# Kernel optimization log

Hardware: AMD Instinct MI355X
Metric: run time of the kernel (lower is better)

The kernel has to match this reference:

```python
import jax, jax.numpy as jnp
import numpy as np

N, C, CI, H, W = 4, 512, 256, 64, 64  # batch, in_channels, inter_channels, spatial
EPS = 1e-5


def conv1x1(x, w, b):
    # x: (N,C,H,W), w: (O,C), b: (O,)
    return jnp.einsum('nchw,oc->nohw', x, w) + b[None, :, None, None]


def setup_inputs() -> dict:
    key = jax.random.key(0)
    ks = jax.random.split(key, 11)
    s = 0.02
    return {
        'x': jax.random.normal(ks[0], (N, C, H, W), dtype=jnp.float32),
        'g_w': jax.random.normal(ks[1], (CI, C), dtype=jnp.float32) * s,
        'g_b': jax.random.normal(ks[2], (CI,), dtype=jnp.float32) * s,
        'theta_w': jax.random.normal(ks[3], (CI, C), dtype=jnp.float32) * s,
        'theta_b': jax.random.normal(ks[4], (CI,), dtype=jnp.float32) * s,
        'phi_w': jax.random.normal(ks[5], (CI, C), dtype=jnp.float32) * s,
        'phi_b': jax.random.normal(ks[6], (CI,), dtype=jnp.float32) * s,
        'wz_w': jax.random.normal(ks[7], (C, CI), dtype=jnp.float32) * s,
        'wz_b': jax.random.normal(ks[8], (C,), dtype=jnp.float32) * s,
        'bn_gamma': jax.random.normal(ks[9], (C,), dtype=jnp.float32) * 0.1 + 1.0,
        'bn_beta': jax.random.normal(ks[10], (C,), dtype=jnp.float32) * 0.1,
    }


def reference(x, g_w, g_b, theta_w, theta_b, phi_w, phi_b, wz_w, wz_b, bn_gamma, bn_beta):
    # NLBlockND.forward_self, mode='embedded', dimension=2, bn_layer=True
    n = x.shape[0]
    L = x.shape[2] * x.shape[3]  # H*W tokens
    g_x = conv1x1(x, g_w, g_b).reshape(n, CI, L)          # (N,Ci,L)
    theta_x = conv1x1(x, theta_w, theta_b).reshape(n, CI, L)
    phi_x = conv1x1(x, phi_w, phi_b).reshape(n, CI, L)
    f = jnp.einsum('ncl,ncm->nlm', theta_x, phi_x)        # (N,L,L) = theta^T @ phi
    f_div_C = jax.nn.softmax(f, axis=-1)
    y = jnp.einsum('nlm,ncm->ncl', f_div_C, g_x)          # (N,Ci,L) = (attn @ g)^T
    y = y.reshape(n, CI, x.shape[2], x.shape[3])
    w_y = conv1x1(y, wz_w, wz_b)                          # (N,C,H,W)
    # BatchNorm2d, training-mode batch statistics (biased variance)
    mean = jnp.mean(w_y, axis=(0, 2, 3), keepdims=True)
    var = jnp.var(w_y, axis=(0, 2, 3), keepdims=True)
    w_y = (w_y - mean) * jax.lax.rsqrt(var + EPS)
    w_y = w_y * bn_gamma[None, :, None, None] + bn_beta[None, :, None, None]
    return w_y + x
```

## Files before the change

### kernel.cpp

```cpp
#include <hip/hip_runtime.h>
#include <hip/hip_bf16.h>
#include <hip/hip_fp16.h>


#define NB    4
#define CDIM  512
#define CIDIM 256
#define LDIM  4096
#define BN_EPS 1e-5f
#define LOG2E 1.4426950408889634f

typedef unsigned short u16;
typedef __attribute__((ext_vector_type(8))) short short8;
typedef __attribute__((ext_vector_type(4))) float f32x4;
typedef __attribute__((ext_vector_type(16))) float f32x16;

#define WY_OFF    0
#define THPH_OFF  8388608
#define G_OFF     12582912
#define Y_OFF     14680064
#define WTS_OFF   16777216
#define BIAS2_OFF 17039360
#define ML_OFF    17039872
#define ST_OFF    17105408

__device__ __forceinline__ u16 f2b(float f) {
    union { float f; unsigned u; } v; v.f = f;
    return (u16)((v.u + 0x7FFFu + ((v.u >> 16) & 1u)) >> 16);
}

__device__ __forceinline__ float b2f(u16 x) {
    return __uint_as_float((unsigned)x << 16);
}

__device__ __forceinline__ unsigned pack2(float a, float b) {
    return (unsigned)f2b(a) | ((unsigned)f2b(b) << 16);
}

__device__ __forceinline__ float fast_exp2(float x) {
#if __has_builtin(__builtin_amdgcn_exp2f)
    return __builtin_amdgcn_exp2f(x);
#else
    float r; asm("v_exp_f32 %0, %1" : "=v"(r) : "v"(x)); return r;
#endif
}

__device__ __forceinline__ void gl_lds16(const u16* g, u16* l) {
    __builtin_amdgcn_global_load_lds(
        (const __attribute__((address_space(1))) void*)g,
        (__attribute__((address_space(3))) void*)l, 16, 0, 0);
}

__global__ void transpose_x(const float* __restrict__ x, u16* __restrict__ xt) {
    __shared__ float tile[32][33];
    int n = blockIdx.z;
    int l0 = blockIdx.x * 32, c0 = blockIdx.y * 32;
    const float* xn = x + (size_t)n * CDIM * LDIM;
    u16* xtn = xt + (size_t)n * LDIM * CDIM;
    int tx = threadIdx.x, ty = threadIdx.y;
#pragma unroll
    for (int k = 0; k < 4; k++)
        tile[ty + 8 * k][tx] = xn[(size_t)(c0 + ty + 8 * k) * LDIM + l0 + tx];
    __syncthreads();
#pragma unroll
    for (int k = 0; k < 4; k++)
        xtn[(size_t)(l0 + ty + 8 * k) * CDIM + c0 + tx] = f2b(tile[tx][ty + 8 * k]);
}

__global__ void cast_w(const float* __restrict__ gw, const float* __restrict__ tw,
                       const float* __restrict__ pw, const float* __restrict__ zw,
                       u16* __restrict__ out,
                       const float* __restrict__ tb, const float* __restrict__ pb,
                       float* __restrict__ bc) {
    int idx = blockIdx.x * 256 + threadIdx.x;
    if (idx < 4 * 131072) {
        int seg = idx >> 17, off = idx & 131071;
        const float* s = (seg == 0) ? gw : (seg == 1) ? tw : (seg == 2) ? pw : zw;
        float v = s[off];
        if (seg == 1) v *= LOG2E;
        out[idx] = f2b(v);
    } else {
        int i = idx - 4 * 131072;
        if (i < 256) bc[i] = tb[i] * LOG2E;
        else if (i < 512) bc[i] = pb[i - 256];
    }
}

template <int BIAS_MODE, bool OUT_BF16>
__global__ __launch_bounds__(256)
void gemm_nt(const u16* __restrict__ A, const u16* __restrict__ B,
             void* __restrict__ Dv, const float* __restrict__ bias,
             int K, int lda, int ldb, int ldd,
             long batchA, long batchB, long batchD) {
    __shared__ __align__(16) u16 As[128 * 32];
    __shared__ __align__(16) u16 Bs[128 * 32];
    int z = blockIdx.z;
    A += (size_t)z * batchA;
    B += (size_t)z * batchB;

    int tid = threadIdx.x, lane = tid & 63, wave = tid >> 6;
    int n0 = blockIdx.x * 128, m0 = blockIdx.y * 128;
    int wr = wave >> 1, wc = wave & 1;

    f32x4 acc[4][4];
#pragma unroll
    for (int i = 0; i < 4; i++)
#pragma unroll
        for (int j = 0; j < 4; j++) acc[i][j] = (f32x4){0.f, 0.f, 0.f, 0.f};

    int sr = wave * 16 + (lane >> 2);
    int ss = ((lane & 3) ^ ((lane >> 2) & 3)) * 8;
    const u16* Ag0 = A + (size_t)(m0 + sr) * lda + ss;
    const u16* Ag1 = A + (size_t)(m0 + 64 + sr) * lda + ss;
    const u16* Bg0 = B + (size_t)(n0 + sr) * ldb + ss;
    const u16* Bg1 = B + (size_t)(n0 + 64 + sr) * ldb + ss;
    u16* Al0 = &As[(wave * 16) * 32];
    u16* Al1 = &As[(64 + wave * 16) * 32];
    u16* Bl0 = &Bs[(wave * 16) * 32];
    u16* Bl1 = &Bs[(64 + wave * 16) * 32];

    int koff = ((lane >> 4) ^ (lane & 3)) * 8;
    int ra = (wr * 64 + (lane & 15)) * 32 + koff;
    int rb = (wc * 64 + (lane & 15)) * 32 + koff;

    for (int k0 = 0; k0 < K; k0 += 32) {
        __syncthreads();
        gl_lds16(Ag0 + k0, Al0);
        gl_lds16(Ag1 + k0, Al1);
        gl_lds16(Bg0 + k0, Bl0);
        gl_lds16(Bg1 + k0, Bl1);
        __syncthreads();

        short8 af[4], bf[4];
#pragma unroll
        for (int mt = 0; mt < 4; mt++) af[mt] = *(const short8*)&As[ra + mt * 16 * 32];
#pragma unroll
        for (int nt = 0; nt < 4; nt++) bf[nt] = *(const short8*)&Bs[rb + nt * 16 * 32];
#pragma unroll
        for (int mt = 0; mt < 4; mt++)
#pragma unroll
            for (int nt = 0; nt < 4; nt++)
                acc[mt][nt] = __builtin_amdgcn_mfma_f32_16x16x32_bf16(
                    af[mt], bf[nt], acc[mt][nt], 0, 0, 0);
    }

#pragma unroll
    for (int mt = 0; mt < 4; mt++) {
        int mg = m0 + wr * 64 + mt * 16 + (lane >> 4) * 4;
#pragma unroll
        for (int nt = 0; nt < 4; nt++) {
            int ng = n0 + wc * 64 + nt * 16 + (lane & 15);
#pragma unroll
            for (int r = 0; r < 4; r++) {
                float v = acc[mt][nt][r];
                if (BIAS_MODE == 1) v += bias[mg + r];
                if (BIAS_MODE == 2) v += bias[ng];
                if (OUT_BF16) {
                    u16* D = (u16*)Dv + (size_t)z * batchD;
                    D[(size_t)(mg + r) * ldd + ng] = f2b(v);
                } else {
                    float* D = (float*)Dv + (size_t)z * batchD;
                    D[(size_t)(mg + r) * ldd + ng] = v;
                }
            }
        }
    }
}

__global__ __launch_bounds__(256, 2)
void flash_attn(const u16* __restrict__ THPH, const u16* __restrict__ G,
                u16* __restrict__ OPB, unsigned* __restrict__ ML4) {
    __shared__ __align__(16) u16 Ks[2][32 * 256];
    __shared__ __align__(16) u16 Vs[2][256 * 32];

    int b = blockIdx.x;
    int n = b & 3;
    int jh = (b >> 2) & 3;
    int qt = b >> 4;
    int q0 = qt * 128;

    const u16* TH = THPH + (size_t)n * LDIM * 512;
    const u16* PH = TH + 256;
    const u16* Gn = G + (size_t)n * LDIM * CIDIM;
    u16* OPh = OPB + ((size_t)jh * NB + n) * CIDIM * LDIM;
    unsigned* MLh = ML4 + ((size_t)jh * NB + n) * LDIM;

    int tid = threadIdx.x, lane = tid & 63, w = tid >> 6;
    int h = lane >> 5, lq = lane & 31, l7 = lane & 7;

    short8 qf[16];
    {
        const u16* qb = TH + (size_t)(q0 + w * 32 + lq) * 512 + h * 8;
#pragma unroll
        for (int c = 0; c < 16; c++) qf[c] = *(const short8*)(qb + c * 16);
    }

    f32x16 o[8];
#pragma unroll
    for (int i = 0; i < 8; i++)
#pragma unroll
        for (int e = 0; e < 16; e++) o[i][e] = 0.f;
    float m = -3e38f, lsum = 0.f;

    int krh = lane >> 5;
    int ksl = lane & 31;
    int vr = lane >> 2;
    int vsl = (lane & 3) ^ ((lane >> 3) & 3);

#define STAGE(bufi, jt_) do {                                                  \
    int j0_ = jh * 1024 + (jt_) * 32;                                          \
    _Pragma("unroll")                                                          \
    for (int i = 0; i < 4; i++) {                                              \
        int r = w * 8 + 2 * i + krh;                                           \
        int s = ksl ^ (r & 7);                                                 \
        gl_lds16(PH + (size_t)(j0_ + r) * 512 + s * 8,                         \
                 &Ks[bufi][(w * 8 + 2 * i) * 256]);                            \
    }                                                                          \
    _Pragma("unroll")                                                          \
    for (int i = 0; i < 4; i++) {                                              \
        int r = w * 64 + 16 * i + vr;                                          \
        gl_lds16(Gn + (size_t)r * LDIM + j0_ + vsl * 8,                        \
                 &Vs[bufi][(w * 64 + 16 * i) * 32]);                           \
    }                                                                          \
} while (0)

    STAGE(0, 0);
    int cur = 0;

#pragma unroll 1
    for (int jt = 0; jt < 32; jt++) {
        __syncthreads();
        if (jt + 1 < 32) STAGE(cur ^ 1, jt + 1);

        const u16* kb = Ks[cur];
        const u16* vb = Vs[cur];

        f32x16 sv;
#pragma unroll
        for (int e = 0; e < 16; e++) sv[e] = 0.f;
#pragma unroll
        for (int c = 0; c < 16; c++) {
            int slot = (c * 2 + h) ^ l7;
            short8 ka = *(const short8*)&kb[lq * 256 + slot * 8];
            sv = __builtin_amdgcn_mfma_f32_32x32x16_bf16(ka, qf[c], sv, 0, 0, 0);
        }

        float tm = sv[0];
#pragma unroll
        for (int r = 1; r < 16; r++) tm = fmaxf(tm, sv[r]);
        tm = fmaxf(tm, __shfl_xor(tm, 32, 64));

        if (!__all(tm <= m + 11.5f)) {
            float mnew = fmaxf(m, tm);
            float al = fast_exp2(m - mnew);
            m = mnew;
            lsum *= al;
#pragma unroll
            for (int i = 0; i < 8; i++)
#pragma unroll
                for (int e = 0; e < 16; e++) o[i][e] *= al;
        }

        float rs = 0.f;
#pragma unroll
        for (int r = 0; r < 16; r++) {
            float p = fast_exp2(sv[r] - m);
            sv[r] = p;
            rs += p;
        }
        lsum += rs + __shfl_xor(rs, 32, 64);

#pragma unroll
        for (int st = 0; st < 2; st++) {
            int r0 = 8 * st;
            float e0 = sv[r0 + 0], e1 = sv[r0 + 1];
            float e2 = sv[r0 + 2], e3 = sv[r0 + 3];
            float e4 = sv[r0 + 4], e5 = sv[r0 + 5];
            float e6 = sv[r0 + 6], e7 = sv[r0 + 7];
            unsigned own_a = h ? pack2(e4, e5) : pack2(e0, e1);
            unsigned own_b = h ? pack2(e6, e7) : pack2(e2, e3);
            unsigned snd_a = h ? pack2(e0, e1) : pack2(e4, e5);
            unsigned snd_b = h ? pack2(e2, e3) : pack2(e6, e7);
            unsigned rcv_a = __shfl_xor(snd_a, 32, 64);
            unsigned rcv_b = __shfl_xor(snd_b, 32, 64);
            union { unsigned u[4]; short8 v; } pf;
            pf.u[0] = h ? rcv_a : own_a;
            pf.u[1] = h ? rcv_b : own_b;
            pf.u[2] = h ? own_a : rcv_a;
            pf.u[3] = h ? own_b : rcv_b;
            int slot = (st * 2 + h) ^ ((lq >> 1) & 3);
#pragma unroll
            for (int cit = 0; cit < 8; cit++) {
                short8 va = *(const short8*)&vb[(cit * 32 + lq) * 32 + slot * 8];
                o[cit] = __builtin_amdgcn_mfma_f32_32x32x16_bf16(va, pf.v, o[cit], 0, 0, 0);
            }
        }
        cur ^= 1;
    }

    int q = q0 + w * 32 + lq;
    if (h == 0) {
        unsigned pm = (unsigned)__half_as_ushort(__float2half(m));
        unsigned pl = (unsigned)__half_as_ushort(__float2half(lsum));
        MLh[q] = pm | (pl << 16);
    }
#pragma unroll
    for (int cit = 0; cit < 8; cit++)
#pragma unroll
        for (int rr = 0; rr < 16; rr++) {
            int ci = cit * 32 + (rr & 3) + 8 * (rr >> 2) + 4 * h;
            OPh[(size_t)ci * LDIM + q] = f2b(o[cit][rr]);
        }
#undef STAGE
}

__global__ void merge_y(const u16* __restrict__ OPB, const unsigned* __restrict__ ML4,
                        u16* __restrict__ Y) {
    __shared__ u16 tile[32][33];
    int nn = blockIdx.z;
    int l0 = blockIdx.x * 32, ci0 = blockIdx.y * 32;
    int tx = threadIdx.x, ty = threadIdx.y;
    int l = l0 + tx;

    float mq[4], lq[4];
#pragma unroll
    for (int q = 0; q < 4; q++) {
        unsigned u = ML4[((size_t)q * NB + nn) * LDIM + l];
        mq[q] = __half2float(__ushort_as_half((unsigned short)(u & 0xffff)));
        lq[q] = __half2float(__ushort_as_half((unsigned short)(u >> 16)));
    }
    float M = fmaxf(fmaxf(mq[0], mq[1]), fmaxf(mq[2], mq[3]));
    float wq[4];
    float den = 0.f;
#pragma unroll
    for (int q = 0; q < 4; q++) {
        wq[q] = fast_exp2(mq[q] - M);
        den += lq[q] * wq[q];
    }
    float inv = 1.f / den;
#pragma unroll
    for (int q = 0; q < 4; q++) wq[q] *= inv;

#pragma unroll
    for (int k = 0; k < 4; k++) {
        int ci = ci0 + ty + 8 * k;
        float acc = 0.f;
#pragma unroll
        for (int q = 0; q < 4; q++)
            acc += b2f(OPB[((size_t)q * NB + nn) * CIDIM * LDIM + (size_t)ci * LDIM + l]) * wq[q];
        tile[ty + 8 * k][tx] = f2b(acc);
    }
    __syncthreads();
    u16* Yn = Y + (size_t)nn * LDIM * CIDIM;
#pragma unroll
    for (int k = 0; k < 4; k++)
        Yn[(size_t)(l0 + ty + 8 * k) * CIDIM + ci0 + tx] = tile[tx][ty + 8 * k];
}

__global__ void bn_stats_kernel(const float* __restrict__ WY, float* __restrict__ stats) {
    int o = blockIdx.x, tid = threadIdx.x, lane = tid & 63, wave = tid >> 6;
    float s = 0.f, s2 = 0.f;
    for (int n = 0; n < NB; n++) {
        const float4* p = (const float4*)(WY + (size_t)(n * CDIM + o) * LDIM);
        for (int i = tid; i < LDIM / 4; i += 256) {
            float4 v = p[i];
            s += v.x + v.y + v.z + v.w;
            s2 += v.x * v.x + v.y * v.y + v.z * v.z + v.w * v.w;
        }
    }
    for (int o2 = 32; o2 > 0; o2 >>= 1) {
        s += __shfl_xor(s, o2, 64);
        s2 += __shfl_xor(s2, o2, 64);
    }
    __shared__ float rs[4], rs2[4];
    if (lane == 0) { rs[wave] = s; rs2[wave] = s2; }
    __syncthreads();
    if (tid == 0) {
        float S = rs[0] + rs[1] + rs[2] + rs[3];
        float S2 = rs2[0] + rs2[1] + rs2[2] + rs2[3];
        const float cnt = (float)(NB * LDIM);
        float mean = S / cnt;
        float var = S2 / cnt - mean * mean;
        stats[o] = mean;
        stats[CDIM + o] = rsqrtf(var + BN_EPS);
    }
}

__global__ void bn_apply_kernel(const float* __restrict__ WY, const float* __restrict__ stats,
                                const float* __restrict__ x,
                                const float* __restrict__ gamma, const float* __restrict__ beta,
                                float* __restrict__ out) {
    int i4 = blockIdx.x * 256 + threadIdx.x;
    int o = (i4 >> 10) & (CDIM - 1);
    float m = stats[o], is = stats[CDIM + o];
    float ga = gamma[o], be = beta[o];
    float4 w = ((const float4*)WY)[i4];
    float4 xv = ((const float4*)x)[i4];
    float4 r;
    r.x = (w.x - m) * is * ga + be + xv.x;
    r.y = (w.y - m) * is * ga + be + xv.y;
    r.z = (w.z - m) * is * ga + be + xv.z;
    r.w = (w.w - m) * is * ga + be + xv.w;
    ((float4*)out)[i4] = r;
}

extern "C" void kernel_launch(void* const* d_in, const int* in_sizes, int n_in,
                              void* d_out, int out_size, void* d_ws, size_t ws_size,
                              hipStream_t stream) {
    const float* x   = (const float*)d_in[0];
    const float* gw  = (const float*)d_in[1];
    const float* gb  = (const float*)d_in[2];
    const float* tw  = (const float*)d_in[3];
    const float* tb  = (const float*)d_in[4];
    const float* pw  = (const float*)d_in[5];
    const float* pb  = (const float*)d_in[6];
    const float* zw  = (const float*)d_in[7];
    const float* zb  = (const float*)d_in[8];
    const float* bng = (const float*)d_in[9];
    const float* bnb = (const float*)d_in[10];
    float* out = (float*)d_out;
    float* ws  = (float*)d_ws;

    float*    WY   = ws + WY_OFF;
    u16*      xT   = (u16*)(ws + WY_OFF);
    u16*      OPB  = (u16*)(ws + WY_OFF);
    u16*      THPH = (u16*)(ws + THPH_OFF);
    u16*      G    = (u16*)(ws + G_OFF);
    u16*      Y    = (u16*)(ws + Y_OFF);
    u16*      WB   = (u16*)(ws + WTS_OFF);
    float*    BC   = ws + BIAS2_OFF;
    unsigned* ML4  = (unsigned*)(ws + ML_OFF);
    float*    ST   = ws + ST_OFF;

    const long LC   = (long)LDIM * CDIM;
    const long LCI  = (long)LDIM * CIDIM;
    const long L512 = (long)LDIM * 512;
    const long CL   = (long)CDIM * LDIM;

    transpose_x<<<dim3(LDIM / 32, CDIM / 32, NB), dim3(32, 8), 0, stream>>>(x, xT);
    cast_w<<<2050, 256, 0, stream>>>(gw, tw, pw, zw, WB, tb, pb, BC);

    gemm_nt<2, true><<<dim3(4, 32, NB), 256, 0, stream>>>(
        xT, WB + 131072, THPH, BC, CDIM, CDIM, CDIM, 512, LC, 0, L512);
    gemm_nt<1, true><<<dim3(32, 2, NB), 256, 0, stream>>>(
        WB, xT, G, gb, CDIM, CDIM, CDIM, LDIM, 0, LC, LCI);

    flash_attn<<<dim3(512), 256, 0, stream>>>(THPH, G, OPB, ML4);
    merge_y<<<dim3(LDIM / 32, CIDIM / 32, NB), dim3(32, 8), 0, stream>>>(OPB, ML4, Y);

    gemm_nt<1, false><<<dim3(32, 4, NB), 256, 0, stream>>>(
        WB + 393216, Y, (void*)WY, zb, CIDIM, CIDIM, CIDIM, LDIM, 0, LCI, CL);

    bn_stats_kernel<<<dim3(CDIM), 256, 0, stream>>>(WY, ST);
    bn_apply_kernel<<<dim3(NB * CDIM * LDIM / 4 / 256), 256, 0, stream>>>(
        WY, ST, x, bng, bnb, out);
}
```

Measured before the change: 280.6 us.

## Double-buffer GEMM LDS tiles and split QK MFMA chain in attention

The projection GEMM now uses two LDS buffers and prefetches the next K-tile while computing on the current one, removing one barrier per iteration. In the attention kernel, the QK^T accumulation is split into two independent MFMA chains that are summed afterwards, which shortens the dependency chain. V fragment loads are also hoisted ahead of the PV MFMAs. The cost is doubled LDS for the GEMM and extra registers for the second accumulator and the V fragments, which may reduce occupancy.

```diff
diff --git a/kernel.cpp b/kernel.cpp
--- a/kernel.cpp
+++ b/kernel.cpp
@@ -92,8 +92,8 @@
              void* __restrict__ Dv, const float* __restrict__ bias,
              int K, int lda, int ldb, int ldd,
              long batchA, long batchB, long batchD) {
-    __shared__ __align__(16) u16 As[128 * 32];
-    __shared__ __align__(16) u16 Bs[128 * 32];
+    __shared__ __align__(16) u16 As[2][128 * 32];
+    __shared__ __align__(16) u16 Bs[2][128 * 32];
     int z = blockIdx.z;
     A += (size_t)z * batchA;
     B += (size_t)z * batchB;
@@ -114,35 +114,40 @@
     const u16* Ag1 = A + (size_t)(m0 + 64 + sr) * lda + ss;
     const u16* Bg0 = B + (size_t)(n0 + sr) * ldb + ss;
     const u16* Bg1 = B + (size_t)(n0 + 64 + sr) * ldb + ss;
-    u16* Al0 = &As[(wave * 16) * 32];
-    u16* Al1 = &As[(64 + wave * 16) * 32];
-    u16* Bl0 = &Bs[(wave * 16) * 32];
-    u16* Bl1 = &Bs[(64 + wave * 16) * 32];
+    int sdst = wave * 16 * 32;
 
     int koff = ((lane >> 4) ^ (lane & 3)) * 8;
     int ra = (wr * 64 + (lane & 15)) * 32 + koff;
     int rb = (wc * 64 + (lane & 15)) * 32 + koff;
 
+#define GSTAGE(bi, k0_) do {                                                   \
+    gl_lds16(Ag0 + (k0_), &As[bi][sdst]);                                      \
+    gl_lds16(Ag1 + (k0_), &As[bi][sdst + 2048]);                               \
+    gl_lds16(Bg0 + (k0_), &Bs[bi][sdst]);                                      \
+    gl_lds16(Bg1 + (k0_), &Bs[bi][sdst + 2048]);                               \
+} while (0)
+
+    GSTAGE(0, 0);
+    int cur = 0;
+
     for (int k0 = 0; k0 < K; k0 += 32) {
         __syncthreads();
-        gl_lds16(Ag0 + k0, Al0);
-        gl_lds16(Ag1 + k0, Al1);
-        gl_lds16(Bg0 + k0, Bl0);
-        gl_lds16(Bg1 + k0, Bl1);
-        __syncthreads();
+        if (k0 + 32 < K) GSTAGE(cur ^ 1, k0 + 32);
 
         short8 af[4], bf[4];
 #pragma unroll
-        for (int mt = 0; mt < 4; mt++) af[mt] = *(const short8*)&As[ra + mt * 16 * 32];
-#pragma unroll
-        for (int nt = 0; nt < 4; nt++) bf[nt] = *(const short8*)&Bs[rb + nt * 16 * 32];
+        for (int mt = 0; mt < 4; mt++) af[mt] = *(const short8*)&As[cur][ra + mt * 512];
+#pragma unroll
+        for (int nt = 0; nt < 4; nt++) bf[nt] = *(const short8*)&Bs[cur][rb + nt * 512];
 #pragma unroll
         for (int mt = 0; mt < 4; mt++)
 #pragma unroll
             for (int nt = 0; nt < 4; nt++)
                 acc[mt][nt] = __builtin_amdgcn_mfma_f32_16x16x32_bf16(
                     af[mt], bf[nt], acc[mt][nt], 0, 0, 0);
-    }
+        cur ^= 1;
+    }
+#undef GSTAGE
 
 #pragma unroll
     for (int mt = 0; mt < 4; mt++) {
@@ -235,15 +240,22 @@
         const u16* kb = Ks[cur];
         const u16* vb = Vs[cur];
 
-        f32x16 sv;
-#pragma unroll
-        for (int e = 0; e < 16; e++) sv[e] = 0.f;
-#pragma unroll
-        for (int c = 0; c < 16; c++) {
+        f32x16 svx, svy;
+#pragma unroll
+        for (int e = 0; e < 16; e++) { svx[e] = 0.f; svy[e] = 0.f; }
+#pragma unroll
+        for (int c = 0; c < 8; c++) {
             int slot = (c * 2 + h) ^ l7;
             short8 ka = *(const short8*)&kb[lq * 256 + slot * 8];
-            sv = __builtin_amdgcn_mfma_f32_32x32x16_bf16(ka, qf[c], sv, 0, 0, 0);
-        }
+            svx = __builtin_amdgcn_mfma_f32_32x32x16_bf16(ka, qf[c], svx, 0, 0, 0);
+        }
+#pragma unroll
+        for (int c = 8; c < 16; c++) {
+            int slot = (c * 2 + h) ^ l7;
+            short8 ka = *(const short8*)&kb[lq * 256 + slot * 8];
+            svy = __builtin_amdgcn_mfma_f32_32x32x16_bf16(ka, qf[c], svy, 0, 0, 0);
+        }
+        f32x16 sv = svx + svy;
 
         float tm = sv[0];
 #pragma unroll
@@ -289,11 +301,13 @@
             pf.u[2] = h ? own_a : rcv_a;
             pf.u[3] = h ? own_b : rcv_b;
             int slot = (st * 2 + h) ^ ((lq >> 1) & 3);
-#pragma unroll
-            for (int cit = 0; cit < 8; cit++) {
-                short8 va = *(const short8*)&vb[(cit * 32 + lq) * 32 + slot * 8];
-                o[cit] = __builtin_amdgcn_mfma_f32_32x32x16_bf16(va, pf.v, o[cit], 0, 0, 0);
-            }
+            short8 va[8];
+#pragma unroll
+            for (int cit = 0; cit < 8; cit++)
+                va[cit] = *(const short8*)&vb[(cit * 32 + lq) * 32 + slot * 8];
+#pragma unroll
+            for (int cit = 0; cit < 8; cit++)
+                o[cit] = __builtin_amdgcn_mfma_f32_32x32x16_bf16(va[cit], pf.v, o[cit], 0, 0, 0);
         }
         cur ^= 1;
     }
```

Result: slower. 300.1 us (+7.0%).
